# Performance work log

Hardware: AMD Instinct MI355X
Metric: run time of the kernel (lower is better)

The kernel has to match this reference:

```python
import jax, jax.numpy as jnp
import numpy as np

P = 8  # patch size hardcoded in FSAS/DFFN
EPS = 1e-5


def conv1x1(x, w):
    # x: [B,C,H,W], w: [Cout,Cin]
    return jnp.einsum('bchw,oc->bohw', x, w)


def dwconv3(x, w):
    # depthwise 3x3, w: [C,1,3,3]
    return jax.lax.conv_general_dilated(
        x, w, window_strides=(1, 1), padding='SAME',
        dimension_numbers=('NCHW', 'OIHW', 'NCHW'),
        feature_group_count=x.shape[1])


def layernorm_c(x, w, b):
    # WithBias LayerNorm over channel dim (torch: b c h w -> b (h w) c, LN over c)
    mu = jnp.mean(x, axis=1, keepdims=True)
    var = jnp.var(x, axis=1, keepdims=True)
    return (x - mu) / jnp.sqrt(var + EPS) * w[None, :, None, None] + b[None, :, None, None]


def to_patches(x):
    # [B,C,H,W] -> [B,C,H/P,W/P,P,P]
    B, C, H, W = x.shape
    return x.reshape(B, C, H // P, P, W // P, P).transpose(0, 1, 2, 4, 3, 5)


def from_patches(xp):
    B, C, h, w, p1, p2 = xp.shape
    return xp.transpose(0, 1, 2, 4, 3, 5).reshape(B, C, h * p1, w * p2)


def fsas(x, w_hidden, dw, norm_w, norm_b, w_out):
    hidden = conv1x1(x, w_hidden)          # [B,6d,H,W]
    qkv = dwconv3(hidden, dw)
    q, k, v = jnp.split(qkv, 3, axis=1)    # each [B,2d,H,W]
    qf = jnp.fft.rfft2(to_patches(q))
    kf = jnp.fft.rfft2(to_patches(k))
    out = jnp.fft.irfft2(qf * kf, s=(P, P))
    out = layernorm_c(from_patches(out), norm_w, norm_b)
    return conv1x1(v * out, w_out)


def dffn(x, w_in, fft_w, dw, w_out):
    x = conv1x1(x, w_in)                   # [B,2h,H,W]
    xf = jnp.fft.rfft2(to_patches(x))
    # fft_w: [2h,1,1,P,P//2+1] broadcasts against [B,2h,h,w,P,P//2+1]
    x = from_patches(jnp.fft.irfft2(xf * fft_w, s=(P, P)))
    x1, x2 = jnp.split(dwconv3(x, dw), 2, axis=1)
    return conv1x1(jax.nn.gelu(x1, approximate=False) * x2, w_out)


def setup_inputs() -> dict:
    key = jax.random.key(0)
    ks = jax.random.split(key, 10)
    d = 48
    h = int(d * 3)  # ffn_expansion_factor=3 -> hidden_features=144
    B, H, W = 2, 256, 256

    def n(k, shape, s=0.05):
        return jax.random.normal(k, shape, jnp.float32) * s

    return {
        'x': jax.random.normal(ks[0], (B, d, H, W), jnp.float32),
        'norm1_w': jnp.ones((d,), jnp.float32),
        'norm1_b': jnp.zeros((d,), jnp.float32),
        'attn_w_hidden': n(ks[1], (6 * d, d)),
        'attn_dw': n(ks[2], (6 * d, 1, 3, 3), 0.2),
        'attn_norm_w': jnp.ones((2 * d,), jnp.float32),
        'attn_norm_b': jnp.zeros((2 * d,), jnp.float32),
        'attn_w_out': n(ks[3], (d, 2 * d)),
        'norm2_w': jnp.ones((d,), jnp.float32),
        'norm2_b': jnp.zeros((d,), jnp.float32),
        'ffn_w_in': n(ks[4], (2 * h, d)),
        'ffn_fft': 1.0 + n(ks[5], (2 * h, 1, 1, P, P // 2 + 1), 0.1),
        'ffn_dw': n(ks[6], (2 * h, 1, 3, 3), 0.2),
        'ffn_w_out': n(ks[7], (d, h)),
    }


def reference(x, norm1_w, norm1_b, attn_w_hidden, attn_dw, attn_norm_w,
              attn_norm_b, attn_w_out, norm2_w, norm2_b, ffn_w_in, ffn_fft,
              ffn_dw, ffn_w_out):
    x = x + fsas(layernorm_c(x, norm1_w, norm1_b),
                 attn_w_hidden, attn_dw, attn_norm_w, attn_norm_b, attn_w_out)
    x = x + dffn(layernorm_c(x, norm2_w, norm2_b),
                 ffn_w_in, ffn_fft, ffn_dw, ffn_w_out)
    return x
```

## Files before the change

kernel.cpp:

```cpp
#include <hip/hip_runtime.h>
#include <hip/hip_bf16.h>
#include <cstddef>


constexpr int HWC = 65536;

typedef short short8 __attribute__((ext_vector_type(8)));
typedef __bf16 bf16x8 __attribute__((ext_vector_type(8)));
typedef float f32x4 __attribute__((ext_vector_type(4)));

__device__ inline unsigned short f2bf(float f) {
  __hip_bfloat16 h = __float2bfloat16(f);
  return *reinterpret_cast<unsigned short*>(&h);
}
__device__ inline float bf2f(unsigned short u) {
  __hip_bfloat16 h;
  *reinterpret_cast<unsigned short*>(&h) = u;
  return __bfloat162float(h);
}

union V8 { uint4 v; unsigned short us[8]; short s[8]; };

__device__ inline void load8f(const unsigned short* p, float* f) {
  V8 u; u.v = *reinterpret_cast<const uint4*>(p);
#pragma unroll
  for (int j = 0; j < 8; j++) f[j] = bf2f(u.us[j]);
}
__device__ inline void store8bf(unsigned short* p, const float* f) {
  V8 u;
#pragma unroll
  for (int j = 0; j < 8; j++) u.us[j] = f2bf(f[j]);
  *reinterpret_cast<uint4*>(p) = u.v;
}

__global__ __launch_bounds__(64) void k_prep_w(
    const float* __restrict__ awh, const float* __restrict__ awo,
    const float* __restrict__ fwi, const float* __restrict__ fwo,
    unsigned short* __restrict__ wp) {
  int row = blockIdx.x, t = threadIdx.x;
  const float* src; int K, KP; unsigned short* dst;
  if (row < 288)      { src = awh + row * 48;        K = 48;  KP = 64;
                        dst = wp + row * 64; }
  else if (row < 336) { int r = row - 288; src = awo + r * 96; K = 96; KP = 96;
                        dst = wp + 18432 + r * 96; }
  else if (row < 624) { int r = row - 336; src = fwi + r * 48; K = 48; KP = 64;
                        dst = wp + 23040 + r * 64; }
  else                { int r = row - 624; src = fwo + r * 144; K = 144; KP = 160;
                        dst = wp + 41472 + r * 160; }
  for (int k = t; k < KP; k += 64) dst[k] = f2bf(k < K ? src[k] : 0.f);
}

template <int M, int K, int KP, int XF, int EPI>
__global__ __launch_bounds__(256) void k_gemm(
    const unsigned short* __restrict__ wb, const void* __restrict__ s1,
    const unsigned short* __restrict__ s2, const float* __restrict__ lnw,
    const float* __restrict__ lnb, const void* __restrict__ res,
    void* __restrict__ out) {
  constexpr int STRIDE = KP + 8;
  constexpr int KS = KP / 32;
  constexpr int NT = (M + 63) / 64;
  __shared__ __align__(16) short Xs[64 * STRIDE];
  __shared__ __align__(16) short Vs[(XF == 2) ? 64 * STRIDE : 4];
  __shared__ float redS[4][64], redS2[4][64], mus[64], invs[64];

  int tid = threadIdx.x;
  unsigned bid = blockIdx.x;
  int b = (int)(bid >> 10);
  int hw0 = (int)(bid & 1023) * 64;

  if (XF == 1) {
    const float* xp = (const float*)s1 + (size_t)b * 48 * HWC + hw0;
    for (int idx = tid; idx < 48 * 16; idx += 256) {
      int c = idx >> 4, colg = (idx & 15) * 4;
      float4 f = *reinterpret_cast<const float4*>(xp + (size_t)c * HWC + colg);
      Xs[(colg + 0) * STRIDE + c] = (short)f2bf(f.x);
      Xs[(colg + 1) * STRIDE + c] = (short)f2bf(f.y);
      Xs[(colg + 2) * STRIDE + c] = (short)f2bf(f.z);
      Xs[(colg + 3) * STRIDE + c] = (short)f2bf(f.w);
    }
  } else if (XF == 2) {
    const unsigned short* up =
        (const unsigned short*)s1 + (size_t)b * 96 * HWC + hw0;
    const unsigned short* vp = s2 + ((size_t)(b * 288 + 192)) * HWC + hw0;
    for (int idx = tid; idx < 96 * 16; idx += 256) {
      int c = idx >> 4, colg = (idx & 15) * 4;
      ushort4 uv = *reinterpret_cast<const ushort4*>(up + (size_t)c * HWC + colg);
      Xs[(colg + 0) * STRIDE + c] = (short)uv.x;
      Xs[(colg + 1) * STRIDE + c] = (short)uv.y;
      Xs[(colg + 2) * STRIDE + c] = (short)uv.z;
      Xs[(colg + 3) * STRIDE + c] = (short)uv.w;
      ushort4 vv = *reinterpret_cast<const ushort4*>(vp + (size_t)c * HWC + colg);
      Vs[(colg + 0) * STRIDE + c] = (short)vv.x;
      Vs[(colg + 1) * STRIDE + c] = (short)vv.y;
      Vs[(colg + 2) * STRIDE + c] = (short)vv.z;
      Vs[(colg + 3) * STRIDE + c] = (short)vv.w;
    }
  } else if (XF == 3) {
    const unsigned short* xp =
        (const unsigned short*)s1 + (size_t)b * 48 * HWC + hw0;
    for (int idx = tid; idx < 48 * 16; idx += 256) {
      int c = idx >> 4, colg = (idx & 15) * 4;
      ushort4 uv = *reinterpret_cast<const ushort4*>(xp + (size_t)c * HWC + colg);
      Xs[(colg + 0) * STRIDE + c] = (short)uv.x;
      Xs[(colg + 1) * STRIDE + c] = (short)uv.y;
      Xs[(colg + 2) * STRIDE + c] = (short)uv.z;
      Xs[(colg + 3) * STRIDE + c] = (short)uv.w;
    }
  } else {
    const unsigned short* p1 =
        (const unsigned short*)s1 + (size_t)b * 96 * HWC + hw0;
    const unsigned short* p2 = s2 + (size_t)b * 48 * HWC + hw0;
    for (int idx = tid; idx < K * 16; idx += 256) {
      int c = idx >> 4, colg = (idx & 15) * 4;
      const unsigned short* p =
          (c < 96) ? (p1 + (size_t)c * HWC + colg)
                   : (p2 + (size_t)(c - 96) * HWC + colg);
      ushort4 uv = *reinterpret_cast<const ushort4*>(p);
      Xs[(colg + 0) * STRIDE + c] = (short)uv.x;
      Xs[(colg + 1) * STRIDE + c] = (short)uv.y;
      Xs[(colg + 2) * STRIDE + c] = (short)uv.z;
      Xs[(colg + 3) * STRIDE + c] = (short)uv.w;
    }
  }

  if constexpr (KP > K) {
    constexpr int PAD = KP - K;
    for (int idx = tid; idx < 64 * PAD; idx += 256) {
      int col = idx / PAD, c = K + (idx % PAD);
      Xs[col * STRIDE + c] = 0;
    }
  }

  if (XF != 0) {
    constexpr int KC = (XF == 2) ? 96 : 48;
    __syncthreads();
    {
      int col = tid & 63, q = tid >> 6;
      float s = 0.f, s2 = 0.f;
      for (int c = q * (KC / 4); c < (q + 1) * (KC / 4); c++) {
        float v = bf2f((unsigned short)Xs[col * STRIDE + c]);
        s += v; s2 += v * v;
      }
      redS[q][col] = s; redS2[q][col] = s2;
    }
    __syncthreads();
    if (tid < 64) {
      float ss = redS[0][tid] + redS[1][tid] + redS[2][tid] + redS[3][tid];
      float ss2 = redS2[0][tid] + redS2[1][tid] + redS2[2][tid] + redS2[3][tid];
      float mu = ss * (1.f / KC);
      float var = ss2 * (1.f / KC) - mu * mu;
      mus[tid] = mu; invs[tid] = rsqrtf(var + 1e-5f);
    }
    __syncthreads();
    for (int idx = tid; idx < KC * 64; idx += 256) {
      int c = idx >> 6, col = idx & 63;
      float v = bf2f((unsigned short)Xs[col * STRIDE + c]);
      v = (v - mus[col]) * invs[col] * lnw[c] + lnb[c];
      if (XF == 2) v *= bf2f((unsigned short)Vs[col * STRIDE + c]);
      Xs[col * STRIDE + c] = (short)f2bf(v);
    }
  }
  __syncthreads();

  int lane = tid & 63, wvi = tid >> 6;
  int quad = lane >> 4, mc = lane & 15;
  int kbase = quad * 8;

  short8 bfr[4][KS];
#pragma unroll
  for (int ns = 0; ns < 4; ns++)
#pragma unroll
    for (int ks = 0; ks < KS; ks++)
      bfr[ns][ks] = *reinterpret_cast<const short8*>(
          Xs + (ns * 16 + mc) * STRIDE + ks * 32 + kbase);

  short* Es = Xs;
#pragma unroll
  for (int t = 0; t < NT; t++) {
    int mb = (wvi + 4 * t) * 16;
    f32x4 accs[4];
    if (mb < M) {
      short8 afr[KS];
#pragma unroll
      for (int ks = 0; ks < KS; ks++)
        afr[ks] = *reinterpret_cast<const short8*>(
            wb + (size_t)(mb + mc) * KP + ks * 32 + kbase);
#pragma unroll
      for (int ns = 0; ns < 4; ns++) {
        f32x4 acc = {0.f, 0.f, 0.f, 0.f};
#pragma unroll
        for (int ks = 0; ks < KS; ks++)
          acc = __builtin_amdgcn_mfma_f32_16x16x32_bf16(
              __builtin_bit_cast(bf16x8, afr[ks]),
              __builtin_bit_cast(bf16x8, bfr[ns][ks]), acc, 0, 0, 0);
        accs[ns] = acc;
      }
    }
    __syncthreads();
    if (mb < M) {
      int chl = wvi * 16 + quad * 4;
#pragma unroll
      for (int ns = 0; ns < 4; ns++)
#pragma unroll
        for (int r = 0; r < 4; r++)
          Es[(chl + r) * 72 + ns * 16 + mc] = (short)f2bf(accs[ns][r]);
    }
    __syncthreads();
#pragma unroll
    for (int i = 0; i < 2; i++) {
      int chl = (tid >> 3) + 32 * i;
      int px0 = (tid & 7) * 8;
      int m = 64 * t + chl;
      if (m < M) {
        V8 ev;
        ev.v = *reinterpret_cast<const uint4*>(Es + chl * 72 + px0);
        size_t off = ((size_t)(b * ((EPI == 0) ? M : 48) + m)) * HWC + hw0 + px0;
        if (EPI == 0) {
          *reinterpret_cast<uint4*>((unsigned short*)out + off) = ev.v;
        } else if (EPI == 1) {
          const float* rp = (const float*)res + off;
          float4 ra = *reinterpret_cast<const float4*>(rp);
          float4 rb = *reinterpret_cast<const float4*>(rp + 4);
          V8 pk;
          pk.us[0] = f2bf(ra.x + bf2f(ev.us[0]));
          pk.us[1] = f2bf(ra.y + bf2f(ev.us[1]));
          pk.us[2] = f2bf(ra.z + bf2f(ev.us[2]));
          pk.us[3] = f2bf(ra.w + bf2f(ev.us[3]));
          pk.us[4] = f2bf(rb.x + bf2f(ev.us[4]));
          pk.us[5] = f2bf(rb.y + bf2f(ev.us[5]));
          pk.us[6] = f2bf(rb.z + bf2f(ev.us[6]));
          pk.us[7] = f2bf(rb.w + bf2f(ev.us[7]));
          *reinterpret_cast<uint4*>((unsigned short*)out + off) = pk.v;
        } else {
          V8 rv;
          rv.v = *reinterpret_cast<const uint4*>((const unsigned short*)res + off);
          float* op = (float*)out + off;
          float4 oa, ob;
          oa.x = bf2f(rv.us[0]) + bf2f(ev.us[0]);
          oa.y = bf2f(rv.us[1]) + bf2f(ev.us[1]);
          oa.z = bf2f(rv.us[2]) + bf2f(ev.us[2]);
          oa.w = bf2f(rv.us[3]) + bf2f(ev.us[3]);
          ob.x = bf2f(rv.us[4]) + bf2f(ev.us[4]);
          ob.y = bf2f(rv.us[5]) + bf2f(ev.us[5]);
          ob.z = bf2f(rv.us[6]) + bf2f(ev.us[6]);
          ob.w = bf2f(rv.us[7]) + bf2f(ev.us[7]);
          *reinterpret_cast<float4*>(op) = oa;
          *reinterpret_cast<float4*>(op + 4) = ob;
        }
      }
    }
  }
}

__global__ __launch_bounds__(256) void k_dwconv3v(
    const unsigned short* __restrict__ in, const float* __restrict__ dw,
    unsigned short* __restrict__ out) {
  int tid = threadIdx.x;
  unsigned bid = blockIdx.x;
  int y0 = (int)(bid & 31) * 8;
  unsigned t = bid >> 5;
  int c = 192 + (int)(t % 96u);
  int b = (int)(t / 96u);
  const unsigned short* ip = in + ((size_t)(b * 288 + c)) * HWC;
  float wv[9];
#pragma unroll
  for (int k = 0; k < 9; k++) wv[k] = dw[c * 9 + k];
  int r = tid >> 5, seg = tid & 31, lane = tid & 63;
  int y = y0 + r;
  float f[3][8];
#pragma unroll
  for (int dy = 0; dy < 3; dy++) {
    int yy = y + dy - 1;
    if (yy >= 0 && yy < 256) {
      load8f(ip + yy * 256 + seg * 8, f[dy]);
    } else {
#pragma unroll
      for (int j = 0; j < 8; j++) f[dy][j] = 0.f;
    }
  }
  float o[8];
#pragma unroll
  for (int dy = 0; dy < 3; dy++) {
    float lv = __shfl(f[dy][7], lane - 1, 64);
    float rv = __shfl(f[dy][0], lane + 1, 64);
    if (seg == 0) lv = 0.f;
    if (seg == 31) rv = 0.f;
#pragma unroll
    for (int j = 0; j < 8; j++) {
      float xl = (j == 0) ? lv : f[dy][j - 1];
      float xr = (j == 7) ? rv : f[dy][j + 1];
      float v = xl * wv[dy * 3] + f[dy][j] * wv[dy * 3 + 1] + xr * wv[dy * 3 + 2];
      o[j] = (dy == 0) ? v : o[j] + v;
    }
  }
  store8bf(out + ((size_t)(b * 288 + c)) * HWC + y * 256 + seg * 8, o);
}

__global__ __launch_bounds__(256) void k_fsas_fused(
    const unsigned short* __restrict__ hid, const float* __restrict__ dw,
    unsigned short* __restrict__ out) {
  __shared__ float qs[8][296];
  __shared__ float kt[8][296];
  int tid = threadIdx.x;
  unsigned bid = blockIdx.x;
  int py = (int)(bid & 31);
  int c = (int)((bid >> 5) % 96u);
  int b = (int)((bid >> 5) / 96u);
  const unsigned short* qp = hid + ((size_t)(b * 288 + c)) * HWC;
  const unsigned short* kp = hid + ((size_t)(b * 288 + 96 + c)) * HWC;
  float w1[9], w2[9];
#pragma unroll
  for (int k = 0; k < 9; k++) {
    w1[k] = dw[c * 9 + k];
    w2[k] = dw[(96 + c) * 9 + k];
  }
  int r = tid >> 5, seg = tid & 31, lane = tid & 63;
  int y = py * 8 + r;
  float f1[3][8], f2[3][8];
#pragma unroll
  for (int dy = 0; dy < 3; dy++) {
    int yy = y + dy - 1;
    if (yy >= 0 && yy < 256) {
      load8f(qp + yy * 256 + seg * 8, f1[dy]);
      load8f(kp + yy * 256 + seg * 8, f2[dy]);
    } else {
#pragma unroll
      for (int j = 0; j < 8; j++) { f1[dy][j] = 0.f; f2[dy][j] = 0.f; }
    }
  }
  float d1[8], d2[8];
#pragma unroll
  for (int j = 0; j < 8; j++) { d1[j] = 0.f; d2[j] = 0.f; }
#pragma unroll
  for (int dy = 0; dy < 3; dy++) {
    float lv1 = __shfl(f1[dy][7], lane - 1, 64);
    float rv1 = __shfl(f1[dy][0], lane + 1, 64);
    float lv2 = __shfl(f2[dy][7], lane - 1, 64);
    float rv2 = __shfl(f2[dy][0], lane + 1, 64);
    if (seg == 0) { lv1 = 0.f; lv2 = 0.f; }
    if (seg == 31) { rv1 = 0.f; rv2 = 0.f; }
#pragma unroll
    for (int j = 0; j < 8; j++) {
      float xl1 = (j == 0) ? lv1 : f1[dy][j - 1];
      float xr1 = (j == 7) ? rv1 : f1[dy][j + 1];
      float xl2 = (j == 0) ? lv2 : f2[dy][j - 1];
      float xr2 = (j == 7) ? rv2 : f2[dy][j + 1];
      d1[j] += xl1 * w1[dy * 3] + f1[dy][j] * w1[dy * 3 + 1] + xr1 * w1[dy * 3 + 2];
      d2[j] += xl2 * w2[dy * 3] + f2[dy][j] * w2[dy * 3 + 1] + xr2 * w2[dy * 3 + 2];
    }
  }
#pragma unroll
  for (int j = 0; j < 8; j++) {
    qs[r][seg * 9 + j] = d1[j];
    kt[r][seg * 9 + j] = d2[j];
  }
  __syncthreads();
  int p = tid >> 3, a = tid & 7;
  float acc[8];
#pragma unroll
  for (int j = 0; j < 8; j++) acc[j] = 0.f;
#pragma unroll
  for (int i = 0; i < 8; i++) {
    float q8[8], k8[8];
#pragma unroll
    for (int j = 0; j < 8; j++) q8[j] = qs[i][p * 9 + j];
    int ar = (a - i) & 7;
#pragma unroll
    for (int j = 0; j < 8; j++) k8[j] = kt[ar][p * 9 + j];
#pragma unroll
    for (int j = 0; j < 8; j++)
#pragma unroll
      for (int bb = 0; bb < 8; bb++) acc[bb] += q8[j] * k8[(bb - j) & 7];
  }
  store8bf(out + ((size_t)(b * 96 + c)) * HWC + (py * 8 + a) * 256 + p * 8,
           acc);
}

__device__ const float c_cos8[8] = {
    1.f, 0.70710678118654752f, 0.f, -0.70710678118654752f,
    -1.f, -0.70710678118654752f, 0.f, 0.70710678118654752f};

__global__ __launch_bounds__(64) void k_make_cmat(
    const float* __restrict__ fftw, unsigned short* __restrict__ cmat) {
  __shared__ float sf[64];
  int c = blockIdx.x;
  int a = threadIdx.x >> 3, b2 = threadIdx.x & 7;
  const float* W = fftw + c * 40;
  float acc = 0.f;
  for (int u = 0; u < 8; u++) {
    for (int v = 0; v < 8; v++) {
      float wv;
      if (v <= 4) {
        if (v == 0 || v == 4)
          wv = 0.5f * (W[u * 5 + v] + W[((8 - u) & 7) * 5 + v]);
        else
          wv = W[u * 5 + v];
      } else {
        wv = W[((8 - u) & 7) * 5 + (8 - v)];
      }
      acc += wv * c_cos8[(u * a + v * b2) & 7];
    }
  }
  sf[threadIdx.x] = acc * (1.f / 64.f);
  __syncthreads();
  unsigned short* cp = cmat + (size_t)c * 4096 + threadIdx.x * 64;
  for (int k8 = 0; k8 < 64; k8 += 8) {
    float v[8];
    int ka = k8 >> 3;
    int ia = ((a - ka) & 7) * 8;
#pragma unroll
    for (int j = 0; j < 8; j++) v[j] = sf[ia + ((b2 - j) & 7)];
    store8bf(cp + k8, v);
  }
}

__global__ __launch_bounds__(256) void k_patchconv_mfma(
    unsigned short* y, const unsigned short* __restrict__ cmat) {
  __shared__ __align__(16) short Bs[32 * 72];
  __shared__ __align__(16) short As[64 * 72];
  int tid = threadIdx.x;
  unsigned bid = blockIdx.x;
  int py = (int)(bid & 31);
  int c = (int)((bid >> 5) % 288u);
  int b = (int)((bid >> 5) / 288u);
  unsigned short* yp = y + ((size_t)(b * 288 + c)) * HWC + py * 2048;
  {
    int rr = tid >> 5, seg = tid & 31;
    *reinterpret_cast<uint4*>(Bs + seg * 72 + rr * 8) =
        *reinterpret_cast<const uint4*>(yp + rr * 256 + seg * 8);
  }
  {
    const unsigned short* cp = cmat + (size_t)c * 4096;
    int m = tid >> 2, kq = (tid & 3) * 16;
    *reinterpret_cast<uint4*>(As + m * 72 + kq) =
        *reinterpret_cast<const uint4*>(cp + m * 64 + kq);
    *reinterpret_cast<uint4*>(As + m * 72 + kq + 8) =
        *reinterpret_cast<const uint4*>(cp + m * 64 + kq + 8);
  }
  __syncthreads();
  int lane = tid & 63, wvi = tid >> 6;
  int quad = lane >> 4, mc = lane & 15;
  int kbase = quad * 8;
  short8 afr[2];
#pragma unroll
  for (int ks = 0; ks < 2; ks++)
    afr[ks] = *reinterpret_cast<const short8*>(
        As + (wvi * 16 + mc) * 72 + ks * 32 + kbase);
#pragma unroll
  for (int nt = 0; nt < 2; nt++) {
    short8 bfr[2];
#pragma unroll
    for (int ks = 0; ks < 2; ks++)
      bfr[ks] = *reinterpret_cast<const short8*>(
          Bs + (nt * 16 + mc) * 72 + ks * 32 + kbase);
    f32x4 acc = {0.f, 0.f, 0.f, 0.f};
#pragma unroll
    for (int ks = 0; ks < 2; ks++)
      acc = __builtin_amdgcn_mfma_f32_16x16x32_bf16(
          __builtin_bit_cast(bf16x8, afr[ks]),
          __builtin_bit_cast(bf16x8, bfr[ks]), acc, 0, 0, 0);
    int p = nt * 16 + mc;
    int m0 = wvi * 16 + quad * 4;
    int a = m0 >> 3, b8 = m0 & 7;
    ushort4 pk;
    pk.x = f2bf(acc[0]); pk.y = f2bf(acc[1]);
    pk.z = f2bf(acc[2]); pk.w = f2bf(acc[3]);
    *reinterpret_cast<ushort4*>(yp + a * 256 + p * 8 + b8) = pk;
  }
}

__global__ __launch_bounds__(256) void k_ffn_gate(
    const unsigned short* __restrict__ z, const float* __restrict__ dwf,
    unsigned short* __restrict__ g1, unsigned short* __restrict__ g2) {
  int tid = threadIdx.x;
  unsigned bid = blockIdx.x;
  int y0 = (int)(bid & 31) * 8;
  unsigned t = bid >> 5;
  int c = (int)(t % 144u);
  int b = (int)(t / 144u);
  const unsigned short* zp1 = z + ((size_t)(b * 288 + c)) * HWC;
  const unsigned short* zp2 = z + ((size_t)(b * 288 + 144 + c)) * HWC;
  float w1[9], w2[9];
#pragma unroll
  for (int k = 0; k < 9; k++) {
    w1[k] = dwf[c * 9 + k];
    w2[k] = dwf[(144 + c) * 9 + k];
  }
  int r = tid >> 5, seg = tid & 31, lane = tid & 63;
  int y = y0 + r;
  float f1[3][8], f2[3][8];
#pragma unroll
  for (int dy = 0; dy < 3; dy++) {
    int yy = y + dy - 1;
    if (yy >= 0 && yy < 256) {
      load8f(zp1 + yy * 256 + seg * 8, f1[dy]);
      load8f(zp2 + yy * 256 + seg * 8, f2[dy]);
    } else {
#pragma unroll
      for (int j = 0; j < 8; j++) { f1[dy][j] = 0.f; f2[dy][j] = 0.f; }
    }
  }
  float d1[8], d2[8];
#pragma unroll
  for (int j = 0; j < 8; j++) { d1[j] = 0.f; d2[j] = 0.f; }
#pragma unroll
  for (int dy = 0; dy < 3; dy++) {
    float lv1 = __shfl(f1[dy][7], lane - 1, 64);
    float rv1 = __shfl(f1[dy][0], lane + 1, 64);
    float lv2 = __shfl(f2[dy][7], lane - 1, 64);
    float rv2 = __shfl(f2[dy][0], lane + 1, 64);
    if (seg == 0) { lv1 = 0.f; lv2 = 0.f; }
    if (seg == 31) { rv1 = 0.f; rv2 = 0.f; }
#pragma unroll
    for (int j = 0; j < 8; j++) {
      float xl1 = (j == 0) ? lv1 : f1[dy][j - 1];
      float xr1 = (j == 7) ? rv1 : f1[dy][j + 1];
      float xl2 = (j == 0) ? lv2 : f2[dy][j - 1];
      float xr2 = (j == 7) ? rv2 : f2[dy][j + 1];
      d1[j] += xl1 * w1[dy * 3] + f1[dy][j] * w1[dy * 3 + 1] + xr1 * w1[dy * 3 + 2];
      d2[j] += xl2 * w2[dy * 3] + f2[dy][j] * w2[dy * 3 + 1] + xr2 * w2[dy * 3 + 2];
    }
  }
  float o[8];
#pragma unroll
  for (int j = 0; j < 8; j++)
    o[j] = 0.5f * d1[j] * (1.f + erff(d1[j] * 0.70710678118654752f)) * d2[j];
  unsigned short* gp = (c < 96)
      ? g1 + ((size_t)(b * 96 + c)) * HWC
      : g2 + ((size_t)(b * 48 + (c - 96))) * HWC;
  store8bf(gp + y * 256 + seg * 8, o);
}

extern "C" void kernel_launch(void* const* d_in, const int* in_sizes, int n_in,
                              void* d_out, int out_size, void* d_ws,
                              size_t ws_size, hipStream_t stream) {
  (void)in_sizes; (void)n_in; (void)out_size; (void)ws_size;
  const float* x   = (const float*)d_in[0];
  const float* n1w = (const float*)d_in[1];
  const float* n1b = (const float*)d_in[2];
  const float* awh = (const float*)d_in[3];
  const float* adw = (const float*)d_in[4];
  const float* anw = (const float*)d_in[5];
  const float* anb = (const float*)d_in[6];
  const float* awo = (const float*)d_in[7];
  const float* n2w = (const float*)d_in[8];
  const float* n2b = (const float*)d_in[9];
  const float* fwi = (const float*)d_in[10];
  const float* fff = (const float*)d_in[11];
  const float* fdw = (const float*)d_in[12];
  const float* fwo = (const float*)d_in[13];

  unsigned short* QKV  = (unsigned short*)d_ws;
  unsigned short* HID  = (unsigned short*)((char*)d_ws + 75497472);
  unsigned short* U    = (unsigned short*)((char*)d_ws + 150994944);
  unsigned short* X1   = (unsigned short*)((char*)d_ws + 176160768);
  unsigned short* G2   = (unsigned short*)((char*)d_ws + 188743680);
  unsigned short* CMAT = G2;
  unsigned short* WP   = (unsigned short*)((char*)d_ws + 201326592);
  unsigned short* WA = WP;
  unsigned short* WO = WP + 18432;
  unsigned short* WI = WP + 23040;
  unsigned short* WF = WP + 41472;

  k_prep_w<<<672, 64, 0, stream>>>(awh, awo, fwi, fwo, WP);
  k_make_cmat<<<288, 64, 0, stream>>>(fff, CMAT);
  k_gemm<288, 48, 64, 1, 0><<<2048, 256, 0, stream>>>(WA, x, nullptr, n1w,
                                                      n1b, nullptr, HID);
  k_dwconv3v<<<2 * 96 * 32, 256, 0, stream>>>(HID, adw, QKV);
  k_fsas_fused<<<2 * 96 * 32, 256, 0, stream>>>(HID, adw, U);
  k_gemm<48, 96, 96, 2, 1><<<2048, 256, 0, stream>>>(WO, U, QKV, anw, anb, x,
                                                     X1);
  k_gemm<288, 48, 64, 3, 0><<<2048, 256, 0, stream>>>(WI, X1, nullptr, n2w,
                                                      n2b, nullptr, QKV);
  k_patchconv_mfma<<<2 * 288 * 32, 256, 0, stream>>>(QKV, CMAT);
  k_ffn_gate<<<2 * 144 * 32, 256, 0, stream>>>(QKV, fdw, U, G2);
  k_gemm<48, 144, 160, 0, 2><<<2048, 256, 0, stream>>>(WF, U, G2, nullptr,
                                                       nullptr, X1,
                                                       (float*)d_out);
}
```

Baseline: 293.2 us.

## Process 64-row strips per block in FSAS fused kernel with one thread per patch

The fused depthwise-conv plus circular patch convolution kernel now handles a 64-row strip (32 patch columns × 8 patch rows) per block instead of one 8-row strip, looping over eight sub-strips for the depthwise conv. Intermediate q/k are stored in shared memory as fp16 with vectorized 16-byte writes. Each thread then computes a whole 8x8 patch circular convolution in registers, which removes the redundant per-thread shared-memory reloads of q. The grid shrinks eightfold to 768 blocks, so each block keeps far more registers and shared memory live, which may hurt occupancy. The fp16 intermediates also lose some precision.

After: 319.3 us. 1.09x slower.

```diff
diff --git a/kernel.cpp b/kernel.cpp
--- a/kernel.cpp
+++ b/kernel.cpp
@@ -8,6 +8,7 @@
 typedef short short8 __attribute__((ext_vector_type(8)));
 typedef __bf16 bf16x8 __attribute__((ext_vector_type(8)));
 typedef float f32x4 __attribute__((ext_vector_type(4)));
+typedef _Float16 f16x8 __attribute__((ext_vector_type(8)));
 
 __device__ inline unsigned short f2bf(float f) {
   __hip_bfloat16 h = __float2bfloat16(f);
@@ -299,13 +300,15 @@
 __global__ __launch_bounds__(256) void k_fsas_fused(
     const unsigned short* __restrict__ hid, const float* __restrict__ dw,
     unsigned short* __restrict__ out) {
-  __shared__ float qs[8][296];
-  __shared__ float kt[8][296];
+  constexpr int LSTR = 264;
+  __shared__ __align__(16) _Float16 qs[64 * LSTR];
+  __shared__ __align__(16) _Float16 kt[64 * LSTR];
   int tid = threadIdx.x;
   unsigned bid = blockIdx.x;
-  int py = (int)(bid & 31);
-  int c = (int)((bid >> 5) % 96u);
-  int b = (int)((bid >> 5) / 96u);
+  int qtr = (int)(bid & 3);
+  int c = (int)((bid >> 2) % 96u);
+  int b = (int)((bid >> 2) / 96u);
+  int y0 = qtr * 64;
   const unsigned short* qp = hid + ((size_t)(b * 288 + c)) * HWC;
   const unsigned short* kp = hid + ((size_t)(b * 288 + 96 + c)) * HWC;
   float w1[9], w2[9];
@@ -315,65 +318,87 @@
     w2[k] = dw[(96 + c) * 9 + k];
   }
   int r = tid >> 5, seg = tid & 31, lane = tid & 63;
-  int y = py * 8 + r;
-  float f1[3][8], f2[3][8];
-#pragma unroll
-  for (int dy = 0; dy < 3; dy++) {
-    int yy = y + dy - 1;
-    if (yy >= 0 && yy < 256) {
-      load8f(qp + yy * 256 + seg * 8, f1[dy]);
-      load8f(kp + yy * 256 + seg * 8, f2[dy]);
-    } else {
-#pragma unroll
-      for (int j = 0; j < 8; j++) { f1[dy][j] = 0.f; f2[dy][j] = 0.f; }
-    }
-  }
-  float d1[8], d2[8];
-#pragma unroll
-  for (int j = 0; j < 8; j++) { d1[j] = 0.f; d2[j] = 0.f; }
-#pragma unroll
-  for (int dy = 0; dy < 3; dy++) {
-    float lv1 = __shfl(f1[dy][7], lane - 1, 64);
-    float rv1 = __shfl(f1[dy][0], lane + 1, 64);
-    float lv2 = __shfl(f2[dy][7], lane - 1, 64);
-    float rv2 = __shfl(f2[dy][0], lane + 1, 64);
-    if (seg == 0) { lv1 = 0.f; lv2 = 0.f; }
-    if (seg == 31) { rv1 = 0.f; rv2 = 0.f; }
+  for (int s = 0; s < 8; s++) {
+    int y = y0 + s * 8 + r;
+    float f1[3][8], f2[3][8];
+#pragma unroll
+    for (int dy = 0; dy < 3; dy++) {
+      int yy = y + dy - 1;
+      if (yy >= 0 && yy < 256) {
+        load8f(qp + yy * 256 + seg * 8, f1[dy]);
+        load8f(kp + yy * 256 + seg * 8, f2[dy]);
+      } else {
+#pragma unroll
+        for (int j = 0; j < 8; j++) { f1[dy][j] = 0.f; f2[dy][j] = 0.f; }
+      }
+    }
+    float d1[8], d2[8];
+#pragma unroll
+    for (int j = 0; j < 8; j++) { d1[j] = 0.f; d2[j] = 0.f; }
+#pragma unroll
+    for (int dy = 0; dy < 3; dy++) {
+      float lv1 = __shfl(f1[dy][7], lane - 1, 64);
+      float rv1 = __shfl(f1[dy][0], lane + 1, 64);
+      float lv2 = __shfl(f2[dy][7], lane - 1, 64);
+      float rv2 = __shfl(f2[dy][0], lane + 1, 64);
+      if (seg == 0) { lv1 = 0.f; lv2 = 0.f; }
+      if (seg == 31) { rv1 = 0.f; rv2 = 0.f; }
+#pragma unroll
+      for (int j = 0; j < 8; j++) {
+        float xl1 = (j == 0) ? lv1 : f1[dy][j - 1];
+        float xr1 = (j == 7) ? rv1 : f1[dy][j + 1];
+        float xl2 = (j == 0) ? lv2 : f2[dy][j - 1];
+        float xr2 = (j == 7) ? rv2 : f2[dy][j + 1];
+        d1[j] += xl1 * w1[dy * 3] + f1[dy][j] * w1[dy * 3 + 1] + xr1 * w1[dy * 3 + 2];
+        d2[j] += xl2 * w2[dy * 3] + f2[dy][j] * w2[dy * 3 + 1] + xr2 * w2[dy * 3 + 2];
+      }
+    }
+    f16x8 t1, t2;
 #pragma unroll
     for (int j = 0; j < 8; j++) {
-      float xl1 = (j == 0) ? lv1 : f1[dy][j - 1];
-      float xr1 = (j == 7) ? rv1 : f1[dy][j + 1];
-      float xl2 = (j == 0) ? lv2 : f2[dy][j - 1];
-      float xr2 = (j == 7) ? rv2 : f2[dy][j + 1];
-      d1[j] += xl1 * w1[dy * 3] + f1[dy][j] * w1[dy * 3 + 1] + xr1 * w1[dy * 3 + 2];
-      d2[j] += xl2 * w2[dy * 3] + f2[dy][j] * w2[dy * 3 + 1] + xr2 * w2[dy * 3 + 2];
-    }
-  }
-#pragma unroll
-  for (int j = 0; j < 8; j++) {
-    qs[r][seg * 9 + j] = d1[j];
-    kt[r][seg * 9 + j] = d2[j];
+      t1[j] = (_Float16)d1[j];
+      t2[j] = (_Float16)d2[j];
+    }
+    int row = s * 8 + r;
+    *reinterpret_cast<f16x8*>(&qs[row * LSTR + seg * 8]) = t1;
+    *reinterpret_cast<f16x8*>(&kt[row * LSTR + seg * 8]) = t2;
   }
   __syncthreads();
-  int p = tid >> 3, a = tid & 7;
-  float acc[8];
-#pragma unroll
-  for (int j = 0; j < 8; j++) acc[j] = 0.f;
+  int pr = tid >> 5, pc = tid & 31;
+  const _Float16* qbase = &qs[(pr * 8) * LSTR + pc * 8];
+  const _Float16* kbase = &kt[(pr * 8) * LSTR + pc * 8];
+  float q[8][8];
 #pragma unroll
   for (int i = 0; i < 8; i++) {
-    float q8[8], k8[8];
-#pragma unroll
-    for (int j = 0; j < 8; j++) q8[j] = qs[i][p * 9 + j];
-    int ar = (a - i) & 7;
-#pragma unroll
-    for (int j = 0; j < 8; j++) k8[j] = kt[ar][p * 9 + j];
-#pragma unroll
-    for (int j = 0; j < 8; j++)
-#pragma unroll
-      for (int bb = 0; bb < 8; bb++) acc[bb] += q8[j] * k8[(bb - j) & 7];
-  }
-  store8bf(out + ((size_t)(b * 96 + c)) * HWC + (py * 8 + a) * 256 + p * 8,
-           acc);
+    f16x8 v = *reinterpret_cast<const f16x8*>(qbase + i * LSTR);
+#pragma unroll
+    for (int j = 0; j < 8; j++) q[i][j] = (float)v[j];
+  }
+  float acc[8][8];
+#pragma unroll
+  for (int a = 0; a < 8; a++)
+#pragma unroll
+    for (int bq = 0; bq < 8; bq++) acc[a][bq] = 0.f;
+#pragma unroll
+  for (int kr = 0; kr < 8; kr++) {
+    f16x8 kv = *reinterpret_cast<const f16x8*>(kbase + kr * LSTR);
+    float k8[8];
+#pragma unroll
+    for (int j = 0; j < 8; j++) k8[j] = (float)kv[j];
+#pragma unroll
+    for (int i = 0; i < 8; i++) {
+      int o = (i + kr) & 7;
+#pragma unroll
+      for (int j = 0; j < 8; j++)
+#pragma unroll
+        for (int bq = 0; bq < 8; bq++)
+          acc[o][bq] += q[i][j] * k8[(bq - j) & 7];
+    }
+  }
+  unsigned short* op =
+      out + ((size_t)(b * 96 + c)) * HWC + (y0 + pr * 8) * 256 + pc * 8;
+#pragma unroll
+  for (int a = 0; a < 8; a++) store8bf(op + a * 256, acc[a]);
 }
 
 __device__ const float c_cos8[8] = {
@@ -567,7 +592,7 @@
   k_gemm<288, 48, 64, 1, 0><<<2048, 256, 0, stream>>>(WA, x, nullptr, n1w,
                                                       n1b, nullptr, HID);
   k_dwconv3v<<<2 * 96 * 32, 256, 0, stream>>>(HID, adw, QKV);
-  k_fsas_fused<<<2 * 96 * 32, 256, 0, stream>>>(HID, adw, U);
+  k_fsas_fused<<<2 * 96 * 4, 256, 0, stream>>>(HID, adw, U);
   k_gemm<48, 96, 96, 2, 1><<<2048, 256, 0, stream>>>(WO, U, QKV, anw, anb, x,
                                                      X1);
   k_gemm<288, 48, 64, 3, 0><<<2048, 256, 0, stream>>>(WI, X1, nullptr, n2w,
```
